# Kernel tuning notes

Measured on AMD Instinct MI355X. Metric: run time of the kernel, lower is better.

The kernel has to match this reference:

```python
import jax, jax.numpy as jnp
import numpy as np

KH, KW = 3, 3  # window_size[1], window_size[2]
FILTERS = 64
CHANNELS = 32
K = KH * KW * CHANNELS


def _extract_patches_valid(x, kh, kw):
    # TF tf.image.extract_patches ordering: (row_offset, col_offset, channel)
    B, H, W, C = x.shape
    Ho, Wo = H - kh + 1, W - kw + 1
    cols = [x[:, i:i + Ho, j:j + Wo, :] for i in range(kh) for j in range(kw)]
    return jnp.concatenate(cols, axis=-1)  # (B, Ho, Wo, kh*kw*C)


def setup_inputs() -> dict:
    key = jax.random.key(0)
    kx, kw = jax.random.split(key)
    x = jax.random.normal(kx, (8, 32, 32, CHANNELS), dtype=jnp.float32)
    # learned weight per __init__: shape (1, 1, 1, K, filters), random_normal init
    w = jax.random.normal(kw, (1, 1, 1, K, FILTERS), dtype=jnp.float32) * 0.05
    return {"x": x, "w": w}


def reference(x, w):
    # patches: (B, Ho, Wo, K)
    patches = _extract_patches_valid(x, KH, KW)
    # broadcast-add against weights: (B, Ho, Wo, K, filters)
    s = patches[..., None] + w[0, 0, 0]  # w[0,0,0]: (K, filters)
    # tropical conv: max over patch axis minus min over patch axis
    return jnp.max(s, axis=3) - jnp.min(s, axis=3)  # (B, Ho, Wo, filters)
```

## Files before the change

### kernel.cpp

```cpp
#include <hip/hip_runtime.h>


#define C_IN 32
#define NF 64
#define H_OUT 30
#define W_OUT 30
#define W_IN 32

static __device__ __forceinline__ float max3f(float a, float b, float c) {
    return fmaxf(fmaxf(a, b), c);
}
static __device__ __forceinline__ float min3f(float a, float b, float c) {
    return fminf(fminf(a, b), c);
}

__global__ __launch_bounds__(512) void tropconv_kernel(
    const float* __restrict__ x,
    const float* __restrict__ w,
    float* __restrict__ out) {
    const int bx = blockIdx.x;
    const int q = bx & 3;
    const int bho = bx >> 2;
    const int b = bho / H_OUT;
    const int ho = bho - b * H_OUT;
    const int tid = threadIdx.x;
    const int lane = tid & 63;
    const int wave = tid >> 6;

    const int col0 = q * 8;
    const int npx = (q == 3) ? 6 : 8;
    const int ncols = (q == 3) ? 8 : 10;

    __shared__ __align__(16) float xs[3 * 10 * C_IN];
    __shared__ float pmx[8][8][NF];
    __shared__ float pmn[8][8][NF];

    {
        const int nf4_row = ncols * (C_IN / 4);
        const int total_f4 = 3 * nf4_row;
        if (tid < total_f4) {
            const int r = tid / nf4_row;
            const int cc = tid - r * nf4_row;
            const float4* __restrict__ src = (const float4*)(
                x + ((size_t)((b * 32 + ho + r) * W_IN + col0)) * C_IN);
            ((float4*)xs)[r * 80 + cc] = src[cc];
        }
    }

    const float* __restrict__ wbase = w + (size_t)(wave * 4) * NF + lane;

    float wc[4];
    #pragma unroll
    for (int cc = 0; cc < 4; ++cc) wc[cc] = wbase[cc * NF];

    __syncthreads();

    float mx[8], mn[8];
    #pragma unroll
    for (int t = 0; t < 8; ++t) { mx[t] = -INFINITY; mn[t] = INFINITY; }

    #pragma unroll
    for (int ij = 0; ij < 9; ++ij) {
        float wn[4];
        if (ij < 8) {
            #pragma unroll
            for (int cc = 0; cc < 4; ++cc)
                wn[cc] = wbase[((ij + 1) * C_IN + cc) * NF];
        }

        const int i = ij / 3;
        const int j = ij - i * 3;
        const float* __restrict__ xrow = xs + (i * 10 + j) * C_IN + wave * 4;

        #pragma unroll
        for (int px = 0; px < 8; ++px) {
            float4 p = *(const float4*)(xrow + px * C_IN);
            float s0 = p.x + wc[0];
            float s1 = p.y + wc[1];
            float s2 = p.z + wc[2];
            float s3 = p.w + wc[3];
            mx[px] = max3f(max3f(s0, s1, s2), s3, mx[px]);
            mn[px] = min3f(min3f(s0, s1, s2), s3, mn[px]);
        }

        #pragma unroll
        for (int cc = 0; cc < 4; ++cc) wc[cc] = wn[cc];
    }

    #pragma unroll
    for (int px = 0; px < 8; ++px) {
        pmx[wave][px][lane] = mx[px];
        pmn[wave][px][lane] = mn[px];
    }
    __syncthreads();

    const int nout = npx * NF;
    if (tid < nout) {
        const int px = tid >> 6;
        const int f = tid & 63;
        float a = fmaxf(fmaxf(fmaxf(pmx[0][px][f], pmx[1][px][f]),
                              fmaxf(pmx[2][px][f], pmx[3][px][f])),
                        fmaxf(fmaxf(pmx[4][px][f], pmx[5][px][f]),
                              fmaxf(pmx[6][px][f], pmx[7][px][f])));
        float m = fminf(fminf(fminf(pmn[0][px][f], pmn[1][px][f]),
                              fminf(pmn[2][px][f], pmn[3][px][f])),
                        fminf(fminf(pmn[4][px][f], pmn[5][px][f]),
                              fminf(pmn[6][px][f], pmn[7][px][f])));
        out[((size_t)bho * W_OUT + (col0 + px)) * NF + f] = a - m;
    }
}

extern "C" void kernel_launch(void* const* d_in, const int* in_sizes, int n_in,
                              void* d_out, int out_size, void* d_ws, size_t ws_size,
                              hipStream_t stream) {
    const float* x = (const float*)d_in[0];
    const float* w = (const float*)d_in[1];
    float* out = (float*)d_out;

    dim3 grid(8 * H_OUT * 4);
    dim3 block(512);
    tropconv_kernel<<<grid, block, 0, stream>>>(x, w, out);
}
```

Measured before the change: 62.75 us.

## Load input patches via scalar s_load into SGPRs instead of LDS staging

Replaces the LDS staging of the input tile and the first __syncthreads with wave-uniform scalar loads (s_load_dwordx4) into SGPRs, double-buffered across the 9 kernel offsets. Since each wave reads the same 4 channels for all pixels, the values are uniform and can be held in scalar registers, which removes LDS traffic and the barrier. Out-of-range columns are clamped to stay in bounds. The risk is higher SGPR pressure, scalar-cache latency exposed by the manual lgkmcnt waits, and the fragility of the inline asm.

```diff
diff --git a/kernel.cpp b/kernel.cpp
--- a/kernel.cpp
+++ b/kernel.cpp
@@ -7,11 +7,21 @@
 #define W_OUT 30
 #define W_IN 32
 
+typedef __attribute__((ext_vector_type(4))) float f32x4;
+
 static __device__ __forceinline__ float max3f(float a, float b, float c) {
     return fmaxf(fmaxf(a, b), c);
 }
 static __device__ __forceinline__ float min3f(float a, float b, float c) {
     return fminf(fminf(a, b), c);
+}
+
+static __device__ __forceinline__ f32x4 sload16(const float* base, unsigned off_bytes) {
+    f32x4 r;
+    asm volatile("s_load_dwordx4 %0, %1, %2"
+                 : "=s"(r)
+                 : "s"(base), "s"(off_bytes));
+    return r;
 }
 
 __global__ __launch_bounds__(512) void tropconv_kernel(
@@ -25,26 +35,22 @@
     const int ho = bho - b * H_OUT;
     const int tid = threadIdx.x;
     const int lane = tid & 63;
-    const int wave = tid >> 6;
+    const int wave = __builtin_amdgcn_readfirstlane(tid >> 6);
 
     const int col0 = q * 8;
     const int npx = (q == 3) ? 6 : 8;
-    const int ncols = (q == 3) ? 8 : 10;
 
-    __shared__ __align__(16) float xs[3 * 10 * C_IN];
     __shared__ float pmx[8][8][NF];
     __shared__ float pmn[8][8][NF];
 
-    {
-        const int nf4_row = ncols * (C_IN / 4);
-        const int total_f4 = 3 * nf4_row;
-        if (tid < total_f4) {
-            const int r = tid / nf4_row;
-            const int cc = tid - r * nf4_row;
-            const float4* __restrict__ src = (const float4*)(
-                x + ((size_t)((b * 32 + ho + r) * W_IN + col0)) * C_IN);
-            ((float4*)xs)[r * 80 + cc] = src[cc];
-        }
+    const float* sbase = x + ((size_t)(b * 32 + ho) * W_IN) * C_IN + wave * 4;
+
+    const int mcc = 31 - col0;
+    unsigned coff[10];
+    #pragma unroll
+    for (int c = 0; c < 10; ++c) {
+        const int cc = (c < mcc) ? c : mcc;
+        coff[c] = (unsigned)((col0 + cc) * C_IN * 4);
     }
 
     const float* __restrict__ wbase = w + (size_t)(wave * 4) * NF + lane;
@@ -53,7 +59,9 @@
     #pragma unroll
     for (int cc = 0; cc < 4; ++cc) wc[cc] = wbase[cc * NF];
 
-    __syncthreads();
+    f32x4 cur[8], nxt[8];
+    #pragma unroll
+    for (int px = 0; px < 8; ++px) cur[px] = sload16(sbase, coff[px]);
 
     float mx[8], mn[8];
     #pragma unroll
@@ -61,6 +69,19 @@
 
     #pragma unroll
     for (int ij = 0; ij < 9; ++ij) {
+        asm volatile("s_waitcnt lgkmcnt(0)"
+                     : "+s"(cur[0]), "+s"(cur[1]), "+s"(cur[2]), "+s"(cur[3]),
+                       "+s"(cur[4]), "+s"(cur[5]), "+s"(cur[6]), "+s"(cur[7]));
+
+        if (ij < 8) {
+            const int i1 = (ij + 1) / 3;
+            const int j1 = (ij + 1) - i1 * 3;
+            const unsigned rowoff = (unsigned)(i1 * W_IN * C_IN * 4);
+            #pragma unroll
+            for (int px = 0; px < 8; ++px)
+                nxt[px] = sload16(sbase, rowoff + coff[j1 + px]);
+        }
+
         float wn[4];
         if (ij < 8) {
             #pragma unroll
@@ -68,13 +89,9 @@
                 wn[cc] = wbase[((ij + 1) * C_IN + cc) * NF];
         }
 
-        const int i = ij / 3;
-        const int j = ij - i * 3;
-        const float* __restrict__ xrow = xs + (i * 10 + j) * C_IN + wave * 4;
-
         #pragma unroll
         for (int px = 0; px < 8; ++px) {
-            float4 p = *(const float4*)(xrow + px * C_IN);
+            const f32x4 p = cur[px];
             float s0 = p.x + wc[0];
             float s1 = p.y + wc[1];
             float s2 = p.z + wc[2];
@@ -83,8 +100,12 @@
             mn[px] = min3f(min3f(s0, s1, s2), s3, mn[px]);
         }
 
-        #pragma unroll
-        for (int cc = 0; cc < 4; ++cc) wc[cc] = wn[cc];
+        if (ij < 8) {
+            #pragma unroll
+            for (int px = 0; px < 8; ++px) cur[px] = nxt[px];
+            #pragma unroll
+            for (int cc = 0; cc < 4; ++cc) wc[cc] = wn[cc];
+        }
     }
 
     #pragma unroll
```

New measurement: 64.93 us. 1.03x slower.

## Reuse each shared-memory pixel load across three kernel columns and interleave partial reductions

Applied to the files above, without the earlier changes.

The main loop now walks the 3 kernel rows. Each of the 10 input columns is loaded from LDS once and applied to up to three output pixels, one per kernel column, instead of reloading it for every (i,j) offset. This cuts LDS reads per row from 24 to 10. Weights for a whole row (12 values) are loaded at once in a non-unrolled loop, replacing the per-offset software prefetch. Max and min partials are stored interleaved as float2, and the final cross-wave reduction reads float4 and writes float2, using fewer threads with wider accesses.

```diff
diff --git a/kernel.cpp b/kernel.cpp
--- a/kernel.cpp
+++ b/kernel.cpp
@@ -32,8 +32,7 @@
     const int ncols = (q == 3) ? 8 : 10;
 
     __shared__ __align__(16) float xs[3 * 10 * C_IN];
-    __shared__ float pmx[8][8][NF];
-    __shared__ float pmn[8][8][NF];
+    __shared__ __align__(16) float pms[8][8][NF][2];
 
     {
         const int nf4_row = ncols * (C_IN / 4);
@@ -47,66 +46,62 @@
         }
     }
 
-    const float* __restrict__ wbase = w + (size_t)(wave * 4) * NF + lane;
-
-    float wc[4];
-    #pragma unroll
-    for (int cc = 0; cc < 4; ++cc) wc[cc] = wbase[cc * NF];
-
     __syncthreads();
 
     float mx[8], mn[8];
     #pragma unroll
     for (int t = 0; t < 8; ++t) { mx[t] = -INFINITY; mn[t] = INFINITY; }
 
-    #pragma unroll
-    for (int ij = 0; ij < 9; ++ij) {
-        float wn[4];
-        if (ij < 8) {
-            #pragma unroll
-            for (int cc = 0; cc < 4; ++cc)
-                wn[cc] = wbase[((ij + 1) * C_IN + cc) * NF];
-        }
+    const float* __restrict__ wrow = w + (size_t)(wave * 4) * NF + lane;
+    const float* xrow = xs + wave * 4;
 
-        const int i = ij / 3;
-        const int j = ij - i * 3;
-        const float* __restrict__ xrow = xs + (i * 10 + j) * C_IN + wave * 4;
+    #pragma unroll 1
+    for (int r = 0; r < 3; ++r) {
+        float wr[12];
+        #pragma unroll
+        for (int t = 0; t < 12; ++t)
+            wr[t] = wrow[((t >> 2) * C_IN + (t & 3)) * NF];
 
         #pragma unroll
-        for (int px = 0; px < 8; ++px) {
-            float4 p = *(const float4*)(xrow + px * C_IN);
-            float s0 = p.x + wc[0];
-            float s1 = p.y + wc[1];
-            float s2 = p.z + wc[2];
-            float s3 = p.w + wc[3];
-            mx[px] = max3f(max3f(s0, s1, s2), s3, mx[px]);
-            mn[px] = min3f(min3f(s0, s1, s2), s3, mn[px]);
+        for (int cc = 0; cc < 10; ++cc) {
+            const float4 p = *(const float4*)(xrow + cc * C_IN);
+            #pragma unroll
+            for (int j = 0; j < 3; ++j) {
+                const int px = cc - j;
+                if (px >= 0 && px < 8) {
+                    float s0 = p.x + wr[j * 4 + 0];
+                    float s1 = p.y + wr[j * 4 + 1];
+                    float s2 = p.z + wr[j * 4 + 2];
+                    float s3 = p.w + wr[j * 4 + 3];
+                    mx[px] = max3f(max3f(s0, s1, s2), s3, mx[px]);
+                    mn[px] = min3f(min3f(s0, s1, s2), s3, mn[px]);
+                }
+            }
         }
-
-        #pragma unroll
-        for (int cc = 0; cc < 4; ++cc) wc[cc] = wn[cc];
+        wrow += 3 * C_IN * NF;
+        xrow += 10 * C_IN;
     }
 
     #pragma unroll
     for (int px = 0; px < 8; ++px) {
-        pmx[wave][px][lane] = mx[px];
-        pmn[wave][px][lane] = mn[px];
+        float2 v; v.x = mx[px]; v.y = mn[px];
+        *(float2*)&pms[wave][px][lane][0] = v;
     }
     __syncthreads();
 
-    const int nout = npx * NF;
-    if (tid < nout) {
-        const int px = tid >> 6;
-        const int f = tid & 63;
-        float a = fmaxf(fmaxf(fmaxf(pmx[0][px][f], pmx[1][px][f]),
-                              fmaxf(pmx[2][px][f], pmx[3][px][f])),
-                        fmaxf(fmaxf(pmx[4][px][f], pmx[5][px][f]),
-                              fmaxf(pmx[6][px][f], pmx[7][px][f])));
-        float m = fminf(fminf(fminf(pmn[0][px][f], pmn[1][px][f]),
-                              fminf(pmn[2][px][f], pmn[3][px][f])),
-                        fminf(fminf(pmn[4][px][f], pmn[5][px][f]),
-                              fminf(pmn[6][px][f], pmn[7][px][f])));
-        out[((size_t)bho * W_OUT + (col0 + px)) * NF + f] = a - m;
+    if (tid < npx * 32) {
+        const int px = tid >> 5;
+        const int fp = tid & 31;
+        float4 v0 = *(const float4*)&pms[0][px][fp * 2][0];
+        float a0 = v0.x, m0 = v0.y, a1 = v0.z, m1 = v0.w;
+        #pragma unroll
+        for (int ww = 1; ww < 8; ++ww) {
+            const float4 v = *(const float4*)&pms[ww][px][fp * 2][0];
+            a0 = fmaxf(a0, v.x); m0 = fminf(m0, v.y);
+            a1 = fmaxf(a1, v.z); m1 = fminf(m1, v.w);
+        }
+        float2 o; o.x = a0 - m0; o.y = a1 - m1;
+        *(float2*)&out[((size_t)bho * W_OUT + (col0 + px)) * NF + fp * 2] = o;
     }
 }
 
```

Result: no change. 63.80 us (+1.7%).
